# Kernel optimization log

Hardware: AMD Instinct MI355X
Metric: run time of the kernel (lower is better)

Reference implementation:

```python
import jax, jax.numpy as jnp
import numpy as np

K = 19  # hardcoded in the original module (pad=int(19/2), reshape to 19x19)


def _conv3x3(x, w, b):
    # x: [B,C,H,W], w: [O,C,3,3], b: [O]
    y = jax.lax.conv_general_dilated(
        x, w, window_strides=(1, 1), padding=[(1, 1), (1, 1)],
        dimension_numbers=("NCHW", "OIHW", "NCHW"))
    return y + b[None, :, None, None]


def _kernel_conv(x, kernels):
    # x: [B,C,H,W]; kernels: [B,361,H,W] flattened as (kh,kw), shared over channels.
    B, C, H, W = x.shape
    pad = K // 2
    # patches: [B, C*K*K, H, W], channel-major ordering (c slowest, then kh, kw)
    patches = jax.lax.conv_general_dilated_patches(
        x, filter_shape=(K, K), window_strides=(1, 1),
        padding=[(pad, pad), (pad, pad)])
    patches = patches.reshape(B, C, K * K, H, W)
    # out[b,c,h,w] = sum_p patches[b,c,p,h,w] * kernels[b,p,h,w]
    return jnp.einsum("bcphw,bphw->bchw", patches, kernels)


def setup_inputs() -> dict:
    key = jax.random.key(0)
    k1, k2, k3, k4, k5, k6 = jax.random.split(key, 6)
    B, in_ch, out_ch, H, W = 2, 16, 16, 128, 128
    inp = {
        "input": jax.random.normal(k1, (B, in_ch, H, W), jnp.float32),
        "kernel": jax.random.normal(k2, (B, K * K, H, W), jnp.float32),
        "w1": jax.random.normal(k3, (out_ch, in_ch, 3, 3), jnp.float32) * (1.0 / np.sqrt(in_ch * 9)),
        "b1": jax.random.normal(k4, (out_ch,), jnp.float32) * 0.01,
        "w2": jax.random.normal(k5, (out_ch, out_ch, 3, 3), jnp.float32) * (1.0 / np.sqrt(out_ch * 9)),
        "b2": jax.random.normal(k6, (out_ch,), jnp.float32) * 0.01,
    }
    return inp


def reference(input, kernel, w1, b1, w2, b2):
    # conv_1: Conv2d(3x3, pad=1) + GELU (torch default = exact erf gelu)
    x = jax.nn.gelu(_conv3x3(input, w1, b1), approximate=False)
    # per-pixel spatially-varying 19x19 convolution
    y = _kernel_conv(x, kernel)
    # conv_2: Conv2d(3x3, pad=1) + Sigmoid
    out = jax.nn.sigmoid(_conv3x3(y, w2, b2))
    return out
```

## Files before the change

### kernel.cpp

```cpp
#include <hip/hip_runtime.h>
#include <math.h>

constexpr int B = 2, C = 16, H = 128, W = 128;
constexpr int HW = H * W;

constexpr int XR = 146, XS = 148, XCH = XR * XS;
constexpr size_t XPAD_ELEMS = (size_t)B * C * XCH;

constexpr int YR = 130, YS = 136, YCH = YR * YS;

__device__ __forceinline__ float4 ld4(const float* p) { return *(const float4*)p; }

__global__ __launch_bounds__(1024) void kpn19(
    const float* __restrict__ xpad,
    const float* __restrict__ kern,
    float* __restrict__ ypad)
{
    __shared__ __align__(16) float xls[4][2][16][84];
    __shared__ float red[3][16][64];

    int tid  = threadIdx.x;
    int lane = tid & 63;
    int wq   = (tid >> 6) & 3;
    int q    = tid >> 8;
    int blk  = blockIdx.x;
    int wb   = blk & 1;
    int h    = (blk >> 1) & 127;
    int b    = blk >> 8;
    int px   = wb * 64 + lane;
    int c0   = wq * 4;

    if (tid < 64) {
        int pl = tid >> 2, i = tid & 3;
        int col = wb ? 132 + i : i;
        ypad[((size_t)(b * C + pl) * YR + (h + 1)) * YS + col] = 0.f;
    }
    if (h == 0 || h == 127) {
        int r = (h == 0) ? 0 : 129;
        for (int f = tid; f < 1088; f += 1024) {
            int pl = f / 68, col = wb * 68 + f % 68;
            ypad[((size_t)(b * C + pl) * YR + r) * YS + col] = 0.f;
        }
    }

    int idx = tid & 255;
    int ma  = idx;
    int mb  = idx + 256;
    bool vb = (mb < 336);
    int ca  = ma / 21, cola = ma % 21;
    int cb  = vb ? mb / 21 : 0, colb = vb ? mb % 21 : 0;
    int kh0 = q * 5;
    int nkh = (q == 3) ? 4 : 5;

    const float* sa = xpad + (size_t)(b * C + ca) * XCH
                      + (size_t)(h + kh0) * XS + wb * 64 + cola * 4;
    const float* sb = xpad + (size_t)(b * C + cb) * XCH
                      + (size_t)(h + kh0) * XS + wb * 64 + colb * 4;

    const float* kp = kern + (size_t)b * 361 * HW + (size_t)h * W + px;

    float a0 = 0.f, a1 = 0.f, a2 = 0.f, a3 = 0.f;

#define STAGE(bufsel)                                                         \
    {                                                                         \
        __builtin_amdgcn_global_load_lds((const void*)sa,                     \
            (void*)(&xls[q][bufsel][0][0] + wq * 256), 16, 0, 0);             \
        if (vb)                                                               \
            __builtin_amdgcn_global_load_lds((const void*)sb,                 \
                (void*)(&xls[q][bufsel][0][0] + 1024 + wq * 256), 16, 0, 0);  \
        sa += XS; sb += XS;                                                   \
    }

    STAGE(0);
    asm volatile("s_waitcnt vmcnt(0)" ::: "memory");
    __syncthreads();

    #pragma unroll
    for (int r = 0; r < 5; ++r) {
        const int cur = r & 1;
        if (r + 1 < nkh) STAGE(cur ^ 1);
        if (r < nkh) {
            int kh = kh0 + r;
            float kv[19];
            const float* kpr = kp + (size_t)(kh * 19) * HW;
            #pragma unroll
            for (int kw = 0; kw < 19; ++kw)
                kv[kw] = kpr[(size_t)kw * HW];
            __builtin_amdgcn_sched_barrier(0);
            #pragma unroll
            for (int kw = 0; kw < 19; ++kw) {
                float k = kv[kw];
                a0 = fmaf(xls[q][cur][c0 + 0][lane + kw], k, a0);
                a1 = fmaf(xls[q][cur][c0 + 1][lane + kw], k, a1);
                a2 = fmaf(xls[q][cur][c0 + 2][lane + kw], k, a2);
                a3 = fmaf(xls[q][cur][c0 + 3][lane + kw], k, a3);
            }
        }
        asm volatile("s_waitcnt vmcnt(0)" ::: "memory");
        __syncthreads();
    }
#undef STAGE

    if (q > 0) {
        red[q - 1][c0 + 0][lane] = a0;
        red[q - 1][c0 + 1][lane] = a1;
        red[q - 1][c0 + 2][lane] = a2;
        red[q - 1][c0 + 3][lane] = a3;
    }
    __syncthreads();
    if (q == 0) {
        #pragma unroll
        for (int j = 0; j < 3; ++j) {
            a0 += red[j][c0 + 0][lane];
            a1 += red[j][c0 + 1][lane];
            a2 += red[j][c0 + 2][lane];
            a3 += red[j][c0 + 3][lane];
        }
        float* yp = ypad + ((size_t)(b * C + c0) * YR + (h + 1)) * YS + (px + 4);
        yp[0]       = a0;
        yp[YCH]     = a1;
        yp[2 * YCH] = a2;
        yp[3 * YCH] = a3;
    }
}

__global__ __launch_bounds__(512) void conv1_gelu(
    const float* __restrict__ in, const float* __restrict__ w1,
    const float* __restrict__ b1, float* __restrict__ xpad)
{
    __shared__ float ws[2304];
    __shared__ float bs[16];
    __shared__ __align__(16) float xs[16][3][128];

    int tid = threadIdx.x;
    for (int i = tid; i < 2304; i += 512) ws[i] = w1[i];
    if (tid < 16) bs[tid] = b1[tid];

    int px  = tid & 127;
    int ocg = tid >> 7;
    int blk = blockIdx.x;
    int h   = blk & 127;
    int b   = blk >> 7;
    int oc0 = ocg * 4;

    if (tid < 320) {
        int j = tid / 20, i = tid % 20;
        int col = (i < 9) ? i : 128 + i;
        xpad[((size_t)(b * C + j) * XR + (h + 9)) * XS + col] = 0.f;
    }
    if (h == 0 || h == 127) {
        int r0 = (h == 0) ? 0 : 137;
        for (int f = tid; f < 16 * 9 * XS; f += 512) {
            int j = f / (9 * XS), rem = f % (9 * XS);
            int r = r0 + rem / XS, col = rem % XS;
            xpad[((size_t)(b * C + j) * XR + r) * XS + col] = 0.f;
        }
    }

    const float4 z4 = make_float4(0.f, 0.f, 0.f, 0.f);
    #pragma unroll
    for (int j = 0; j < 3; ++j) {
        int m = tid + j * 512;
        int ic = m / 96, rem = m - ic * 96, r = rem >> 5, qq = rem & 31;
        int row = h + r - 1;
        float4 v = ((unsigned)row < 128u)
                 ? ld4(in + ((size_t)(b * C + ic) * H + row) * W + qq * 4) : z4;
        *(float4*)&xs[ic][r][qq * 4] = v;
    }
    __syncthreads();

    bool wm = (px > 0), wp = (px < 127);
    float a0 = 0.f, a1 = 0.f, a2 = 0.f, a3 = 0.f;

    #pragma unroll 1
    for (int ic = 0; ic < 16; ++ic) {
        float t[9];
        #pragma unroll
        for (int r = 0; r < 3; ++r) {
            t[r * 3 + 0] = wm ? xs[ic][r][px - 1] : 0.f;
            t[r * 3 + 1] = xs[ic][r][px];
            t[r * 3 + 2] = wp ? xs[ic][r][px + 1] : 0.f;
        }
        #pragma unroll
        for (int j = 0; j < 4; ++j) {
            const float* wp9 = ws + (oc0 + j) * 144 + ic * 9;
            float s = fmaf(wp9[0], t[0], fmaf(wp9[1], t[1], fmaf(wp9[2], t[2],
                      fmaf(wp9[3], t[3], fmaf(wp9[4], t[4], fmaf(wp9[5], t[5],
                      fmaf(wp9[6], t[6], fmaf(wp9[7], t[7], wp9[8] * t[8]))))))));
            if (j == 0) a0 += s; else if (j == 1) a1 += s;
            else if (j == 2) a2 += s; else a3 += s;
        }
    }

    float* xp = xpad + ((size_t)(b * C + oc0) * XR + (h + 9)) * XS + (px + 9);
    float v;
    v = a0 + bs[oc0 + 0]; xp[0]       = 0.5f * v * (1.0f + erff(v * 0.70710678f));
    v = a1 + bs[oc0 + 1]; xp[XCH]     = 0.5f * v * (1.0f + erff(v * 0.70710678f));
    v = a2 + bs[oc0 + 2]; xp[2 * XCH] = 0.5f * v * (1.0f + erff(v * 0.70710678f));
    v = a3 + bs[oc0 + 3]; xp[3 * XCH] = 0.5f * v * (1.0f + erff(v * 0.70710678f));
}

__global__ __launch_bounds__(512) void conv2_sig(
    const float* __restrict__ ypad, const float* __restrict__ w2,
    const float* __restrict__ b2, float* __restrict__ out)
{
    __shared__ float ws[2304];
    __shared__ float bs[16];
    __shared__ __align__(16) float ys[16][3][136];

    int tid = threadIdx.x;
    for (int i = tid; i < 2304; i += 512) ws[i] = w2[i];
    if (tid < 16) bs[tid] = b2[tid];

    int px  = tid & 127;
    int ocg = tid >> 7;
    int blk = blockIdx.x;
    int h   = blk & 127;
    int b   = blk >> 7;
    int oc0 = ocg * 4;

    #pragma unroll
    for (int j = 0; j < 4; ++j) {
        int m = tid + j * 512;
        if (m < 1632) {
            int ic = m / 102, rem = m - ic * 102, r = rem / 34, qq = rem % 34;
            float4 v = ld4(ypad + ((size_t)(b * C + ic) * YR + (h + r)) * YS + qq * 4);
            *(float4*)&ys[ic][r][qq * 4] = v;
        }
    }
    __syncthreads();

    float a0 = 0.f, a1 = 0.f, a2 = 0.f, a3 = 0.f;

    #pragma unroll 1
    for (int ic = 0; ic < 16; ++ic) {
        float t[9];
        #pragma unroll
        for (int r = 0; r < 3; ++r) {
            t[r * 3 + 0] = ys[ic][r][px + 3];
            t[r * 3 + 1] = ys[ic][r][px + 4];
            t[r * 3 + 2] = ys[ic][r][px + 5];
        }
        #pragma unroll
        for (int j = 0; j < 4; ++j) {
            const float* wp9 = ws + (oc0 + j) * 144 + ic * 9;
            float s = fmaf(wp9[0], t[0], fmaf(wp9[1], t[1], fmaf(wp9[2], t[2],
                      fmaf(wp9[3], t[3], fmaf(wp9[4], t[4], fmaf(wp9[5], t[5],
                      fmaf(wp9[6], t[6], fmaf(wp9[7], t[7], wp9[8] * t[8]))))))));
            if (j == 0) a0 += s; else if (j == 1) a1 += s;
            else if (j == 2) a2 += s; else a3 += s;
        }
    }

    float* op = out + ((size_t)(b * C + oc0) * H + h) * W + px;
    float v;
    v = a0 + bs[oc0 + 0]; op[0]      = 1.0f / (1.0f + expf(-v));
    v = a1 + bs[oc0 + 1]; op[HW]     = 1.0f / (1.0f + expf(-v));
    v = a2 + bs[oc0 + 2]; op[2 * HW] = 1.0f / (1.0f + expf(-v));
    v = a3 + bs[oc0 + 3]; op[3 * HW] = 1.0f / (1.0f + expf(-v));
}

extern "C" void kernel_launch(void* const* d_in, const int* in_sizes, int n_in,
                              void* d_out, int out_size, void* d_ws, size_t ws_size,
                              hipStream_t stream)
{
    const float* input  = (const float*)d_in[0];
    const float* kernel = (const float*)d_in[1];
    const float* w1     = (const float*)d_in[2];
    const float* b1     = (const float*)d_in[3];
    const float* w2     = (const float*)d_in[4];
    const float* b2     = (const float*)d_in[5];
    float* out = (float*)d_out;

    float* xpad = (float*)d_ws;
    float* ypad = xpad + XPAD_ELEMS;

    conv1_gelu<<<256, 512, 0, stream>>>(input, w1, b1, xpad);
    kpn19<<<512, 1024, 0, stream>>>(xpad, kernel, ypad);
    conv2_sig<<<256, 512, 0, stream>>>(ypad, w2, b2, out);
}
```

Baseline: 53.10 us.

## Remap kpn19 threads to one channel by four pixels with float4 loads

Changes the thread mapping in the per-pixel 19x19 kernel. Each thread now computes 4 adjacent pixels of one channel instead of 1 pixel across 4 channels. Kernel weights are read as float4 and the shared-memory x window is held in registers (6 float4). Reduction and output stores are vectorized as float4. In exchange, each kernel weight is loaded by 16 threads (one per channel), where before one load fed 4 channels, so global/L2 kernel traffic rises. The aim is fewer LDS reads and wider global accesses.

```diff
diff --git a/kernel.cpp b/kernel.cpp
--- a/kernel.cpp
+++ b/kernel.cpp
@@ -10,6 +10,10 @@
 constexpr int YR = 130, YS = 136, YCH = YR * YS;
 
 __device__ __forceinline__ float4 ld4(const float* p) { return *(const float4*)p; }
+
+#define XC(A, I)                                                             \
+  (((I) & 3) == 0 ? A[(I) >> 2].x : ((I) & 3) == 1 ? A[(I) >> 2].y           \
+   : ((I) & 3) == 2 ? A[(I) >> 2].z : A[(I) >> 2].w)
 
 __global__ __launch_bounds__(1024) void kpn19(
     const float* __restrict__ xpad,
@@ -17,18 +21,20 @@
     float* __restrict__ ypad)
 {
     __shared__ __align__(16) float xls[4][2][16][84];
-    __shared__ float red[3][16][64];
+    __shared__ __align__(16) float red[3][16][64];
 
     int tid  = threadIdx.x;
     int lane = tid & 63;
     int wq   = (tid >> 6) & 3;
     int q    = tid >> 8;
+    int idx  = tid & 255;
+    int pq   = idx & 15;
+    int ch   = idx >> 4;
     int blk  = blockIdx.x;
     int wb   = blk & 1;
     int h    = (blk >> 1) & 127;
     int b    = blk >> 8;
-    int px   = wb * 64 + lane;
-    int c0   = wq * 4;
+    int w0   = wb * 64;
 
     if (tid < 64) {
         int pl = tid >> 2, i = tid & 3;
@@ -43,7 +49,6 @@
         }
     }
 
-    int idx = tid & 255;
     int ma  = idx;
     int mb  = idx + 256;
     bool vb = (mb < 336);
@@ -53,13 +58,13 @@
     int nkh = (q == 3) ? 4 : 5;
 
     const float* sa = xpad + (size_t)(b * C + ca) * XCH
-                      + (size_t)(h + kh0) * XS + wb * 64 + cola * 4;
+                      + (size_t)(h + kh0) * XS + w0 + cola * 4;
     const float* sb = xpad + (size_t)(b * C + cb) * XCH
-                      + (size_t)(h + kh0) * XS + wb * 64 + colb * 4;
-
-    const float* kp = kern + (size_t)b * 361 * HW + (size_t)h * W + px;
-
-    float a0 = 0.f, a1 = 0.f, a2 = 0.f, a3 = 0.f;
+                      + (size_t)(h + kh0) * XS + w0 + colb * 4;
+
+    const float* kp4 = kern + (size_t)b * 361 * HW + (size_t)h * W + w0 + pq * 4;
+
+    float4 acc = make_float4(0.f, 0.f, 0.f, 0.f);
 
 #define STAGE(bufsel)                                                         \
     {                                                                         \
@@ -81,19 +86,29 @@
         if (r + 1 < nkh) STAGE(cur ^ 1);
         if (r < nkh) {
             int kh = kh0 + r;
-            float kv[19];
-            const float* kpr = kp + (size_t)(kh * 19) * HW;
+            const float* kpr = kp4 + (size_t)(kh * 19) * HW;
+            const float* xb_ = &xls[q][cur][ch][pq * 4];
+            float4 xw[6];
             #pragma unroll
-            for (int kw = 0; kw < 19; ++kw)
-                kv[kw] = kpr[(size_t)kw * HW];
-            __builtin_amdgcn_sched_barrier(0);
+            for (int t = 0; t < 6; ++t) xw[t] = ld4(xb_ + 4 * t);
             #pragma unroll
-            for (int kw = 0; kw < 19; ++kw) {
-                float k = kv[kw];
-                a0 = fmaf(xls[q][cur][c0 + 0][lane + kw], k, a0);
-                a1 = fmaf(xls[q][cur][c0 + 1][lane + kw], k, a1);
-                a2 = fmaf(xls[q][cur][c0 + 2][lane + kw], k, a2);
-                a3 = fmaf(xls[q][cur][c0 + 3][lane + kw], k, a3);
+            for (int kb = 0; kb < 5; ++kb) {
+                const int nk = (kb == 4) ? 3 : 4;
+                float4 kv4[4];
+                #pragma unroll
+                for (int j = 0; j < 4; ++j)
+                    if (j < nk) kv4[j] = ld4(kpr + (size_t)(kb * 4 + j) * HW);
+                __builtin_amdgcn_sched_barrier(0);
+                #pragma unroll
+                for (int j = 0; j < 4; ++j)
+                    if (j < nk) {
+                        const int kw = kb * 4 + j;
+                        float4 kq = kv4[j];
+                        acc.x = fmaf(XC(xw, kw + 0), kq.x, acc.x);
+                        acc.y = fmaf(XC(xw, kw + 1), kq.y, acc.y);
+                        acc.z = fmaf(XC(xw, kw + 2), kq.z, acc.z);
+                        acc.w = fmaf(XC(xw, kw + 3), kq.w, acc.w);
+                    }
             }
         }
         asm volatile("s_waitcnt vmcnt(0)" ::: "memory");
@@ -101,26 +116,16 @@
     }
 #undef STAGE
 
-    if (q > 0) {
-        red[q - 1][c0 + 0][lane] = a0;
-        red[q - 1][c0 + 1][lane] = a1;
-        red[q - 1][c0 + 2][lane] = a2;
-        red[q - 1][c0 + 3][lane] = a3;
-    }
+    if (q > 0) *(float4*)&red[q - 1][ch][pq * 4] = acc;
     __syncthreads();
     if (q == 0) {
         #pragma unroll
         for (int j = 0; j < 3; ++j) {
-            a0 += red[j][c0 + 0][lane];
-            a1 += red[j][c0 + 1][lane];
-            a2 += red[j][c0 + 2][lane];
-            a3 += red[j][c0 + 3][lane];
-        }
-        float* yp = ypad + ((size_t)(b * C + c0) * YR + (h + 1)) * YS + (px + 4);
-        yp[0]       = a0;
-        yp[YCH]     = a1;
-        yp[2 * YCH] = a2;
-        yp[3 * YCH] = a3;
+            float4 rv = ld4(&red[j][ch][pq * 4]);
+            acc.x += rv.x; acc.y += rv.y; acc.z += rv.z; acc.w += rv.w;
+        }
+        float* yp = ypad + ((size_t)(b * C + ch) * YR + (h + 1)) * YS + (w0 + pq * 4 + 4);
+        *(float4*)yp = acc;
     }
 }
 
```

After: 121.4 us. 2.29x slower.
